# Kernel tuning notes

Measured on AMD Instinct MI355X. Metric: run time of the kernel, lower is better.

Reference implementation:

```python
import jax, jax.numpy as jnp
import numpy as np

N_ITER = 100
EPS = 1e-12


def _corr(x, k):
    # x: [C,H,W], k: [kh,kw]; per-channel 'same' cross-correlation, zero padding
    C = x.shape[0]
    kern = jnp.broadcast_to(k, (C, 1) + k.shape)
    return jax.lax.conv_general_dilated(
        x[None], kern, window_strides=(1, 1), padding='SAME',
        feature_group_count=C,
        dimension_numbers=('NCHW', 'OIHW', 'NCHW'))[0]


def _corr_t(x, k):
    # adjoint of zero-padded 'same' correlation = correlation with flipped kernel
    return _corr(x, k[::-1, ::-1])


def _A(x, kernel, reg_kernels, w2):
    # A x = K^T K x + sum_i w_i^2 R_i^T R_i x
    out = _corr_t(_corr(x, kernel), kernel)
    for i in range(reg_kernels.shape[0]):  # small fixed number of reg kernels
        rk = reg_kernels[i]
        out = out + w2[i] * _corr_t(_corr(x, rk), rk)
    return out


def setup_inputs() -> dict:
    key = jax.random.key(0)
    k1, k2, k3, k4 = jax.random.split(key, 4)
    image = jax.random.uniform(k1, (3, 768, 768), dtype=jnp.float32)
    kernel = jax.random.uniform(k2, (15, 15), dtype=jnp.float32)
    kernel = kernel / jnp.sum(kernel)  # normalized blur PSF
    reg_kernels = jax.random.normal(k3, (2, 5, 5), dtype=jnp.float32)
    reg_kernel_weights = jax.random.uniform(
        k4, (2,), dtype=jnp.float32, minval=1e-6, maxval=1.0)
    return {'image': image, 'kernel': kernel, 'reg_kernels': reg_kernels,
            'reg_kernel_weights': reg_kernel_weights}


def reference(image, kernel, reg_kernels, reg_kernel_weights):
    w2 = reg_kernel_weights ** 2
    # CG init: x0 = image, b = image, solve A x = K^T b
    KTb = _corr_t(image, kernel)
    r0 = KTb - _A(image, kernel, reg_kernels, w2)
    xrp0 = jnp.stack([image, r0, r0])  # [3, C, H, W]: x, r, p

    def body(xrp, _):
        x, r, p = xrp[0], xrp[1], xrp[2]
        Ap = _A(p, kernel, reg_kernels, w2)
        rtr = jnp.sum(r * r, axis=(1, 2), keepdims=True)      # per-channel [C,1,1]
        ptAp = jnp.sum(p * Ap, axis=(1, 2), keepdims=True)
        alpha = rtr / (ptAp + EPS)
        x_new = x + alpha * p
        r_new = r - alpha * Ap
        beta = jnp.sum(r_new * r_new, axis=(1, 2), keepdims=True) / (rtr + EPS)
        p_new = r_new + beta * p
        return jnp.stack([x_new, r_new, p_new]), None

    xrp, _ = jax.lax.scan(jax.checkpoint(body), xrp0, None, length=N_ITER)
    return xrp
```

## Files before the change

kernel.cpp:

```cpp
#include <hip/hip_runtime.h>

#define EPS 1e-12f

constexpr int H = 768, W = 768, C = 3;
constexpr int HW = H * W;
constexpr int CHW = C * HW;

constexpr int NSLOT = 16;
constexpr int SSTR = 16;
constexpr int SCALSZ = NSLOT * SSTR;

constexpr int SPW = 100, SPH = 60;
constexpr int S0W = 84;
constexpr int S1W = 76, S1H = 36;
constexpr int UBUF = SPH * SPW;

constexpr int ESPH = 44;
constexpr int ET0H = 30;
constexpr int ES1H = 20;
constexpr int ELDS = ESPH * SPW + 2 * ES1H * S1W;
constexpr int IPW = 92, IPH = 60;
constexpr int NEDGE = 136;

__device__ __forceinline__ float block_reduce_256(float v, float* redbuf) {
    #pragma unroll
    for (int off = 32; off > 0; off >>= 1) v += __shfl_down(v, off, 64);
    const int tid = threadIdx.x;
    if ((tid & 63) == 0) redbuf[tid >> 6] = v;
    __syncthreads();
    return redbuf[0] + redbuf[1] + redbuf[2] + redbuf[3];
}

__device__ __forceinline__ float sum_slots(const float* base, int c) {
    float s = 0.f;
    #pragma unroll
    for (int k = 0; k < NSLOT; ++k) s += base[k * SSTR + c];
    return s;
}

__global__ void tap_prep_k(const float* __restrict__ k15, const float* __restrict__ rks,
                           const float* __restrict__ rw, float* __restrict__ taps) {
    const int tid = threadIdx.x;
    if (tid < 240) {
        const int i = tid >> 4, j = tid & 15;
        taps[tid]       = (j < 15) ? k15[i * 15 + j] : 0.f;
        taps[240 + tid] = (j < 15) ? k15[(14 - i) * 15 + (14 - j)] : 0.f;
    }
    if (tid < 80) {
        const int kk = tid / 40, rem = tid % 40, i = rem >> 3, j = rem & 7;
        taps[480 + tid] = (j < 5) ? rks[kk * 25 + i * 5 + j] : 0.f;
        taps[560 + tid] = (j < 5) ? rks[kk * 25 + (4 - i) * 5 + (4 - j)] : 0.f;
    }
    const float w20 = rw[0] * rw[0], w21 = rw[1] * rw[1];
    if (tid == 0) { taps[1684] = w20; taps[1685] = w21; }
    for (int t = tid; t < 29 * 36; t += 256) {
        const int uy = t / 36, ux = t - uy * 36;
        float s = 0.f;
        if (ux < 29) {
            const int dy = uy - 14, dx = ux - 14;
            for (int sy = 0; sy < 15; ++sy) {
                const int ty = sy + dy;
                if ((unsigned)ty >= 15u) continue;
                for (int sx = 0; sx < 15; ++sx) {
                    const int tx = sx + dx;
                    if ((unsigned)tx < 15u) s += k15[sy * 15 + sx] * k15[ty * 15 + tx];
                }
            }
            if (dy >= -4 && dy <= 4 && dx >= -4 && dx <= 4) {
                float q0 = 0.f, q1 = 0.f;
                for (int sy = 0; sy < 5; ++sy) {
                    const int ty = sy + dy;
                    if ((unsigned)ty >= 5u) continue;
                    for (int sx = 0; sx < 5; ++sx) {
                        const int tx = sx + dx;
                        if ((unsigned)tx >= 5u) continue;
                        q0 += rks[sy * 5 + sx] * rks[ty * 5 + tx];
                        q1 += rks[25 + sy * 5 + sx] * rks[25 + ty * 5 + tx];
                    }
                }
                s += w20 * q0 + w21 * q1;
            }
        }
        taps[640 + t] = s;
    }
}

__global__ __launch_bounds__(256) void prologue_k(
    const float* __restrict__ img, const float* __restrict__ taps,
    float* __restrict__ outR, float* __restrict__ outP, float* __restrict__ outX,
    float* __restrict__ red)
{
    __shared__ __align__(16) float ub[UBUF];
    __shared__ __align__(16) float st1[S1H * S1W];
    __shared__ __align__(16) float st2[S1H * S1W];
    __shared__ float redbuf[4];

    const float* kt   = taps;
    const float* ktf  = taps + 240;
    const float* rkt  = taps + 480;
    const float* rktf = taps + 560;
    const float w02 = taps[1684], w12 = taps[1685];

    const int c = blockIdx.z;
    const int bx = blockIdx.x * 64, by = blockIdx.y * 32;
    const int tid = threadIdx.x;
    const float* inC = img + c * HW;

    for (int t = tid; t < SPH * 96; t += 256) {
        const int ly = t / 96, lx = t - ly * 96;
        const int gy = by - 14 + ly, gx = bx - 14 + lx;
        float v = 0.f;
        if ((unsigned)gy < (unsigned)H && (unsigned)gx < (unsigned)W) v = inC[gy * W + gx];
        ub[ly * SPW + lx] = v;
    }
    __syncthreads();

    const int oy = tid >> 3;
    const int ox = (tid & 7) << 3;

    {
        const int s0 = tid, s1i = tid + 256;
        const int row0 = s0 / 9, c0 = (s0 - row0 * 9) << 3;
        const int row1 = s1i / 9, c1 = (s1i - row1 * 9) << 3;
        const bool v1 = (s1i < 324);
        float b0[8], c0a[8], b1[8], c1a[8];
        #pragma unroll
        for (int k = 0; k < 8; ++k) { b0[k] = 0.f; c0a[k] = 0.f; b1[k] = 0.f; c1a[k] = 0.f; }
        #pragma unroll 1
        for (int i = 0; i < 5; ++i) {
            float kb[8], kc[8];
            #pragma unroll
            for (int q = 0; q < 2; ++q) {
                *(float4*)(kb + 4 * q) = *(const float4*)(rkt + i * 8 + 4 * q);
                *(float4*)(kc + 4 * q) = *(const float4*)(rkt + 40 + i * 8 + 4 * q);
            }
            {
                const float* rp = ub + (row0 + 10 + i) * SPW + c0 + 8;
                float seg[16];
                #pragma unroll
                for (int q = 0; q < 4; ++q) *(float4*)(seg + 4 * q) = *(const float4*)(rp + 4 * q);
                #pragma unroll
                for (int j = 0; j < 5; ++j)
                    #pragma unroll
                    for (int k = 0; k < 8; ++k) {
                        b0[k]  = fmaf(seg[j + k + 2], kb[j], b0[k]);
                        c0a[k] = fmaf(seg[j + k + 2], kc[j], c0a[k]);
                    }
            }
            if (v1) {
                const float* rp = ub + (row1 + 10 + i) * SPW + c1 + 8;
                float seg[16];
                #pragma unroll
                for (int q = 0; q < 4; ++q) *(float4*)(seg + 4 * q) = *(const float4*)(rp + 4 * q);
                #pragma unroll
                for (int j = 0; j < 5; ++j)
                    #pragma unroll
                    for (int k = 0; k < 8; ++k) {
                        b1[k]  = fmaf(seg[j + k + 2], kb[j], b1[k]);
                        c1a[k] = fmaf(seg[j + k + 2], kc[j], c1a[k]);
                    }
            }
        }
        {
            const int gy = by - 2 + row0, gxb = bx - 2 + c0;
            #pragma unroll
            for (int k = 0; k < 8; ++k)
                if (((unsigned)gy >= (unsigned)H) || ((unsigned)(gxb + k) >= (unsigned)W)) { b0[k] = 0.f; c0a[k] = 0.f; }
            float* o1 = st1 + row0 * S1W + c0;
            float* o2 = st2 + row0 * S1W + c0;
            *(float4*)(o1) = make_float4(b0[0], b0[1], b0[2], b0[3]);
            *(float4*)(o1 + 4) = make_float4(b0[4], b0[5], b0[6], b0[7]);
            *(float4*)(o2) = make_float4(c0a[0], c0a[1], c0a[2], c0a[3]);
            *(float4*)(o2 + 4) = make_float4(c0a[4], c0a[5], c0a[6], c0a[7]);
        }
        if (v1) {
            const int gy = by - 2 + row1, gxb = bx - 2 + c1;
            #pragma unroll
            for (int k = 0; k < 8; ++k)
                if (((unsigned)gy >= (unsigned)H) || ((unsigned)(gxb + k) >= (unsigned)W)) { b1[k] = 0.f; c1a[k] = 0.f; }
            float* o1 = st1 + row1 * S1W + c1;
            float* o2 = st2 + row1 * S1W + c1;
            *(float4*)(o1) = make_float4(b1[0], b1[1], b1[2], b1[3]);
            *(float4*)(o1 + 4) = make_float4(b1[4], b1[5], b1[6], b1[7]);
            *(float4*)(o2) = make_float4(c1a[0], c1a[1], c1a[2], c1a[3]);
            *(float4*)(o2 + 4) = make_float4(c1a[4], c1a[5], c1a[6], c1a[7]);
        }
    }

    float pctr[8];
    {
        const float* ctr = ub + (oy + 14) * SPW + ox + 14;
        #pragma unroll
        for (int k = 0; k < 8; ++k) pctr[k] = ctr[k];
    }

    float vimg[8];
    #pragma unroll
    for (int k = 0; k < 8; ++k) vimg[k] = 0.f;
    #pragma unroll 1
    for (int i = 0; i < 15; ++i) {
        const float* rowp = ub + (oy + 7 + i) * SPW + ox + 4;
        float seg[28];
        #pragma unroll
        for (int q = 0; q < 7; ++q) *(float4*)(seg + 4 * q) = *(const float4*)(rowp + 4 * q);
        float kv[16];
        #pragma unroll
        for (int q = 0; q < 4; ++q) *(float4*)(kv + 4 * q) = *(const float4*)(ktf + i * 16 + 4 * q);
        #pragma unroll
        for (int j = 0; j < 15; ++j)
            #pragma unroll
            for (int k = 0; k < 8; ++k) vimg[k] = fmaf(seg[j + k + 3], kv[j], vimg[k]);
    }

    const int s0 = tid, s1i = tid + 256;
    const int row0 = s0 / 10, ca0 = (s0 - row0 * 10) << 3;
    const int row1 = s1i / 10, ca1 = (s1i - row1 * 10) << 3;
    const bool av1 = (s1i < 460);
    float a0[8], a1[8];
    #pragma unroll
    for (int k = 0; k < 8; ++k) { a0[k] = 0.f; a1[k] = 0.f; }
    #pragma unroll 1
    for (int i = 0; i < 15; ++i) {
        float kv[16];
        #pragma unroll
        for (int q = 0; q < 4; ++q) *(float4*)(kv + 4 * q) = *(const float4*)(kt + i * 16 + 4 * q);
        {
            const float* rp = ub + (row0 + i) * SPW + ca0;
            float seg[24];
            #pragma unroll
            for (int q = 0; q < 6; ++q) *(float4*)(seg + 4 * q) = *(const float4*)(rp + 4 * q);
            #pragma unroll
            for (int j = 0; j < 15; ++j)
                #pragma unroll
                for (int k = 0; k < 8; ++k) a0[k] = fmaf(seg[j + k], kv[j], a0[k]);
        }
        if (av1) {
            const float* rp = ub + (row1 + i) * SPW + ca1;
            float seg[24];
            #pragma unroll
            for (int q = 0; q < 6; ++q) *(float4*)(seg + 4 * q) = *(const float4*)(rp + 4 * q);
            #pragma unroll
            for (int j = 0; j < 15; ++j)
                #pragma unroll
                for (int k = 0; k < 8; ++k) a1[k] = fmaf(seg[j + k], kv[j], a1[k]);
        }
    }
    {
        const int gy = by - 7 + row0, gxb = bx - 7 + ca0;
        #pragma unroll
        for (int k = 0; k < 8; ++k)
            if (((unsigned)gy >= (unsigned)H) || ((unsigned)(gxb + k) >= (unsigned)W)) a0[k] = 0.f;
    }
    if (av1) {
        const int gy = by - 7 + row1, gxb = bx - 7 + ca1;
        #pragma unroll
        for (int k = 0; k < 8; ++k)
            if (((unsigned)gy >= (unsigned)H) || ((unsigned)(gxb + k) >= (unsigned)W)) a1[k] = 0.f;
    }
    __syncthreads();
    {
        float* o = ub + row0 * S0W + ca0;
        *(float4*)(o) = make_float4(a0[0], a0[1], a0[2], a0[3]);
        *(float4*)(o + 4) = make_float4(a0[4], a0[5], a0[6], a0[7]);
    }
    if (av1) {
        float* o = ub + row1 * S0W + ca1;
        *(float4*)(o) = make_float4(a1[0], a1[1], a1[2], a1[3]);
        *(float4*)(o + 4) = make_float4(a1[4], a1[5], a1[6], a1[7]);
    }
    __syncthreads();

    float acc[8];
    #pragma unroll
    for (int k = 0; k < 8; ++k) acc[k] = 0.f;
    #pragma unroll 1
    for (int i = 0; i < 15; ++i) {
        float kv[16];
        #pragma unroll
        for (int q = 0; q < 4; ++q) *(float4*)(kv + 4 * q) = *(const float4*)(ktf + i * 16 + 4 * q);
        const float* rp = ub + (oy + i) * S0W + ox;
        float seg[24];
        #pragma unroll
        for (int q = 0; q < 6; ++q) *(float4*)(seg + 4 * q) = *(const float4*)(rp + 4 * q);
        #pragma unroll
        for (int j = 0; j < 15; ++j)
            #pragma unroll
            for (int k = 0; k < 8; ++k) acc[k] = fmaf(seg[j + k], kv[j], acc[k]);
    }
    float accB[8], accC[8];
    #pragma unroll
    for (int k = 0; k < 8; ++k) { accB[k] = 0.f; accC[k] = 0.f; }
    #pragma unroll 1
    for (int i = 0; i < 5; ++i) {
        float kb[8], kc[8];
        #pragma unroll
        for (int q = 0; q < 2; ++q) {
            *(float4*)(kb + 4 * q) = *(const float4*)(rktf + i * 8 + 4 * q);
            *(float4*)(kc + 4 * q) = *(const float4*)(rktf + 40 + i * 8 + 4 * q);
        }
        const float* r1p = st1 + (oy + i) * S1W + ox;
        const float* r2p = st2 + (oy + i) * S1W + ox;
        float sA[12], sB[12];
        #pragma unroll
        for (int q = 0; q < 3; ++q) *(float4*)(sA + 4 * q) = *(const float4*)(r1p + 4 * q);
        #pragma unroll
        for (int q = 0; q < 3; ++q) *(float4*)(sB + 4 * q) = *(const float4*)(r2p + 4 * q);
        #pragma unroll
        for (int j = 0; j < 5; ++j)
            #pragma unroll
            for (int k = 0; k < 8; ++k) {
                accB[k] = fmaf(sA[j + k], kb[j], accB[k]);
                accC[k] = fmaf(sB[j + k], kc[j], accC[k]);
            }
    }

    float v[8];
    #pragma unroll
    for (int k = 0; k < 8; ++k) v[k] = vimg[k] - (acc[k] + w02 * accB[k] + w12 * accC[k]);

    const int g = c * HW + (by + oy) * W + bx + ox;
    *(float4*)(outR + g)     = make_float4(v[0], v[1], v[2], v[3]);
    *(float4*)(outR + g + 4) = make_float4(v[4], v[5], v[6], v[7]);
    *(float4*)(outP + g)     = make_float4(v[0], v[1], v[2], v[3]);
    *(float4*)(outP + g + 4) = make_float4(v[4], v[5], v[6], v[7]);
    *(float4*)(outX + g)     = make_float4(pctr[0], pctr[1], pctr[2], pctr[3]);
    *(float4*)(outX + g + 4) = make_float4(pctr[4], pctr[5], pctr[6], pctr[7]);
    float local = 0.f;
    #pragma unroll
    for (int k = 0; k < 8; ++k) local += v[k] * v[k];
    const float tot = block_reduce_256(local, redbuf);
    if (tid == 0) {
        const int bid = blockIdx.y * gridDim.x + blockIdx.x;
        atomicAdd(red + (bid & (NSLOT - 1)) * SSTR + c, tot);
    }
}

template <bool FIRST>
__global__ __launch_bounds__(256) void stepA_k(
    const float* __restrict__ pold, const float* __restrict__ rvec,
    const float* __restrict__ taps,
    float* __restrict__ Apnew, float* __restrict__ pnew,
    const float* __restrict__ rtrI, const float* __restrict__ rtrIm1,
    float* __restrict__ ptapI)
{
    __shared__ __align__(16) float lds[ELDS];
    __shared__ float redbuf[4];
    const int c = blockIdx.z;
    const int tid = threadIdx.x;
    const int bid = blockIdx.x;

    float beta = 0.f;
    if (!FIRST) beta = sum_slots(rtrI, c) / (sum_slots(rtrIm1, c) + EPS);

    float S1 = 0.f;

    if (bid < NEDGE) {
        float* ub  = lds;
        float* st1 = lds + ESPH * SPW;
        float* st2 = st1 + ES1H * S1W;
        const float* kt   = taps;
        const float* ktf  = taps + 240;
        const float* rkt  = taps + 480;
        const float* rktf = taps + 560;
        const float w02 = taps[1684], w12 = taps[1685];

        const int e = bid >> 1, half = bid & 1;
        int tbx, tby;
        { if (e < 12)      { tbx = e;      tby = 0; }
          else if (e < 24) { tbx = e - 12; tby = 23; }
          else if (e < 46) { tbx = 0;      tby = 1 + (e - 24); }
          else             { tbx = 11;     tby = 1 + (e - 46); } }
        const int bx = tbx * 64, by = tby * 32 + half * 16;

        for (int s = tid; s < ESPH * 96; s += 256) {
            const int ly = s / 96, lx = s - ly * 96;
            const int gy = by - 14 + ly, gx = bx - 14 + lx;
            float pe = 0.f;
            if ((unsigned)gy < (unsigned)H && (unsigned)gx < (unsigned)W) {
                const int g = c * HW + gy * W + gx;
                const float pv = pold[g];
                if (FIRST) pe = pv;
                else {
                    pe = fmaf(beta, pv, rvec[g]);
                    if (ly >= 14 && ly < 30 && lx >= 14 && lx < 78) pnew[g] = pe;
                }
            }
            ub[ly * SPW + lx] = pe;
        }
        __syncthreads();

        const int oy2 = tid >> 4;
        const int ox2 = (tid & 15) << 2;

        {
            const int row0 = tid / 9, c0 = (tid - (tid / 9) * 9) << 3;
            const bool act = (tid < 180);
            float b0[8], c0a[8];
            #pragma unroll
            for (int k = 0; k < 8; ++k) { b0[k] = 0.f; c0a[k] = 0.f; }
            if (act) {
                #pragma unroll 1
                for (int i = 0; i < 5; ++i) {
                    float kb[8], kc[8];
                    #pragma unroll
                    for (int q = 0; q < 2; ++q) {
                        *(float4*)(kb + 4 * q) = *(const float4*)(rkt + i * 8 + 4 * q);
                        *(float4*)(kc + 4 * q) = *(const float4*)(rkt + 40 + i * 8 + 4 * q);
                    }
                    const float* rp = ub + (row0 + 10 + i) * SPW + c0 + 8;
                    float seg[16];
                    #pragma unroll
                    for (int q = 0; q < 4; ++q) *(float4*)(seg + 4 * q) = *(const float4*)(rp + 4 * q);
                    #pragma unroll
                    for (int j = 0; j < 5; ++j)
                        #pragma unroll
                        for (int k = 0; k < 8; ++k) {
                            b0[k]  = fmaf(seg[j + k + 2], kb[j], b0[k]);
                            c0a[k] = fmaf(seg[j + k + 2], kc[j], c0a[k]);
                        }
                }
                const int gy = by - 2 + row0, gxb = bx - 2 + c0;
                #pragma unroll
                for (int k = 0; k < 8; ++k)
                    if (((unsigned)gy >= (unsigned)H) || ((unsigned)(gxb + k) >= (unsigned)W)) { b0[k] = 0.f; c0a[k] = 0.f; }
                float* o1 = st1 + row0 * S1W + c0;
                float* o2 = st2 + row0 * S1W + c0;
                *(float4*)(o1) = make_float4(b0[0], b0[1], b0[2], b0[3]);
                *(float4*)(o1 + 4) = make_float4(b0[4], b0[5], b0[6], b0[7]);
                *(float4*)(o2) = make_float4(c0a[0], c0a[1], c0a[2], c0a[3]);
                *(float4*)(o2 + 4) = make_float4(c0a[4], c0a[5], c0a[6], c0a[7]);
            }
        }

        float pctr[4];
        {
            const float* ctr = ub + (oy2 + 14) * SPW + ox2 + 14;
            #pragma unroll
            for (int k = 0; k < 4; ++k) pctr[k] = ctr[k];
        }

        const int s0 = tid, s1i = tid + 256;
        const int row0 = s0 / 10, ca0 = (s0 - row0 * 10) << 3;
        const int row1 = s1i / 10, ca1 = (s1i - row1 * 10) << 3;
        const bool av1 = (s1i < 300);
        float a0[8], a1[8];
        #pragma unroll
        for (int k = 0; k < 8; ++k) { a0[k] = 0.f; a1[k] = 0.f; }
        #pragma unroll 1
        for (int i = 0; i < 15; ++i) {
            float kv[16];
            #pragma unroll
            for (int q = 0; q < 4; ++q) *(float4*)(kv + 4 * q) = *(const float4*)(kt + i * 16 + 4 * q);
            {
                const float* rp = ub + (row0 + i) * SPW + ca0;
                float seg[24];
                #pragma unroll
                for (int q = 0; q < 6; ++q) *(float4*)(seg + 4 * q) = *(const float4*)(rp + 4 * q);
                #pragma unroll
                for (int j = 0; j < 15; ++j)
                    #pragma unroll
                    for (int k = 0; k < 8; ++k) a0[k] = fmaf(seg[j + k], kv[j], a0[k]);
            }
            if (av1) {
                const float* rp = ub + (row1 + i) * SPW + ca1;
                float seg[24];
                #pragma unroll
                for (int q = 0; q < 6; ++q) *(float4*)(seg + 4 * q) = *(const float4*)(rp + 4 * q);
                #pragma unroll
                for (int j = 0; j < 15; ++j)
                    #pragma unroll
                    for (int k = 0; k < 8; ++k) a1[k] = fmaf(seg[j + k], kv[j], a1[k]);
            }
        }
        {
            const int gy = by - 7 + row0, gxb = bx - 7 + ca0;
            #pragma unroll
            for (int k = 0; k < 8; ++k)
                if (((unsigned)gy >= (unsigned)H) || ((unsigned)(gxb + k) >= (unsigned)W)) a0[k] = 0.f;
        }
        if (av1) {
            const int gy = by - 7 + row1, gxb = bx - 7 + ca1;
            #pragma unroll
            for (int k = 0; k < 8; ++k)
                if (((unsigned)gy >= (unsigned)H) || ((unsigned)(gxb + k) >= (unsigned)W)) a1[k] = 0.f;
        }
        __syncthreads();
        {
            float* o = ub + row0 * S0W + ca0;
            *(float4*)(o) = make_float4(a0[0], a0[1], a0[2], a0[3]);
            *(float4*)(o + 4) = make_float4(a0[4], a0[5], a0[6], a0[7]);
        }
        if (av1) {
            float* o = ub + row1 * S0W + ca1;
            *(float4*)(o) = make_float4(a1[0], a1[1], a1[2], a1[3]);
            *(float4*)(o + 4) = make_float4(a1[4], a1[5], a1[6], a1[7]);
        }
        __syncthreads();

        float acc[4];
        #pragma unroll
        for (int k = 0; k < 4; ++k) acc[k] = 0.f;
        #pragma unroll 1
        for (int i = 0; i < 15; ++i) {
            float kv[16];
            #pragma unroll
            for (int q = 0; q < 4; ++q) *(float4*)(kv + 4 * q) = *(const float4*)(ktf + i * 16 + 4 * q);
            const float* rp = ub + (oy2 + i) * S0W + ox2;
            float seg[20];
            #pragma unroll
            for (int q = 0; q < 5; ++q) *(float4*)(seg + 4 * q) = *(const float4*)(rp + 4 * q);
            #pragma unroll
            for (int j = 0; j < 15; ++j)
                #pragma unroll
                for (int k = 0; k < 4; ++k) acc[k] = fmaf(seg[j + k], kv[j], acc[k]);
        }
        float accB[4], accC[4];
        #pragma unroll
        for (int k = 0; k < 4; ++k) { accB[k] = 0.f; accC[k] = 0.f; }
        #pragma unroll 1
        for (int i = 0; i < 5; ++i) {
            float kb[8], kc[8];
            #pragma unroll
            for (int q = 0; q < 2; ++q) {
                *(float4*)(kb + 4 * q) = *(const float4*)(rktf + i * 8 + 4 * q);
                *(float4*)(kc + 4 * q) = *(const float4*)(rktf + 40 + i * 8 + 4 * q);
            }
            const float* r1p = st1 + (oy2 + i) * S1W + ox2;
            const float* r2p = st2 + (oy2 + i) * S1W + ox2;
            float sA[8], sB[8];
            #pragma unroll
            for (int q = 0; q < 2; ++q) *(float4*)(sA + 4 * q) = *(const float4*)(r1p + 4 * q);
            #pragma unroll
            for (int q = 0; q < 2; ++q) *(float4*)(sB + 4 * q) = *(const float4*)(r2p + 4 * q);
            #pragma unroll
            for (int j = 0; j < 5; ++j)
                #pragma unroll
                for (int k = 0; k < 4; ++k) {
                    accB[k] = fmaf(sA[j + k], kb[j], accB[k]);
                    accC[k] = fmaf(sB[j + k], kc[j], accC[k]);
                }
        }

        float v[4];
        #pragma unroll
        for (int k = 0; k < 4; ++k) v[k] = acc[k] + w02 * accB[k] + w12 * accC[k];

        const int g = c * HW + (by + oy2) * W + bx + ox2;
        *(float4*)(Apnew + g) = make_float4(v[0], v[1], v[2], v[3]);
        #pragma unroll
        for (int k = 0; k < 4; ++k) S1 += pctr[k] * v[k];
    } else {
        const float* tk = taps + 640;
        const int b = bid - NEDGE;
        const int bx = 64 + (b % 10) * 64, by = 32 + (b / 10) * 32;
        const int gy0 = by - 14, gx0 = bx - 14;

        for (int s = tid; s < IPH * IPW; s += 256) {
            const int ly = s / IPW, lx = s - ly * IPW;
            const int g = c * HW + (gy0 + ly) * W + (gx0 + lx);
            const float pv = pold[g];
            float pe;
            if (FIRST) pe = pv;
            else {
                pe = fmaf(beta, pv, rvec[g]);
                if (ly >= 14 && ly < 46 && lx >= 14 && lx < 78) pnew[g] = pe;
            }
            lds[s] = pe;
        }
        __syncthreads();

        const int ox = (tid & 15) << 2;
        const int o0 = (tid >> 4) << 1;

        float a0[4], a1[4];
        #pragma unroll
        for (int k = 0; k < 4; ++k) { a0[k] = 0.f; a1[k] = 0.f; }
        {
            const float* rp = lds + o0 * IPW + ox;
            float seg[32];
            #pragma unroll
            for (int q = 0; q < 8; ++q) *(float4*)(seg + 4 * q) = *(const float4*)(rp + 4 * q);
            #pragma unroll
            for (int j = 0; j < 29; ++j) {
                const float kv = tk[j];
                #pragma unroll
                for (int k = 0; k < 4; ++k) a0[k] = fmaf(seg[j + k], kv, a0[k]);
            }
        }
        #pragma unroll 1
        for (int d = 1; d <= 28; ++d) {
            const float* rp = lds + (o0 + d) * IPW + ox;
            float seg[32];
            #pragma unroll
            for (int q = 0; q < 8; ++q) *(float4*)(seg + 4 * q) = *(const float4*)(rp + 4 * q);
            const float* kr0 = tk + d * 36;
            const float* kr1 = kr0 - 36;
            #pragma unroll
            for (int j = 0; j < 29; ++j) {
                const float kv0 = kr0[j], kv1 = kr1[j];
                #pragma unroll
                for (int k = 0; k < 4; ++k) {
                    a0[k] = fmaf(seg[j + k], kv0, a0[k]);
                    a1[k] = fmaf(seg[j + k], kv1, a1[k]);
                }
            }
        }
        {
            const float* rp = lds + (o0 + 29) * IPW + ox;
            float seg[32];
            #pragma unroll
            for (int q = 0; q < 8; ++q) *(float4*)(seg + 4 * q) = *(const float4*)(rp + 4 * q);
            const float* kr1 = tk + 28 * 36;
            #pragma unroll
            for (int j = 0; j < 29; ++j) {
                const float kv = kr1[j];
                #pragma unroll
                for (int k = 0; k < 4; ++k) a1[k] = fmaf(seg[j + k], kv, a1[k]);
            }
        }

        const int gbase = c * HW + (by + o0) * W + bx + ox;
        const float* c0p = lds + (o0 + 14) * IPW + ox + 14;
        const float* c1p = c0p + IPW;
        *(float4*)(Apnew + gbase)     = make_float4(a0[0], a0[1], a0[2], a0[3]);
        *(float4*)(Apnew + gbase + W) = make_float4(a1[0], a1[1], a1[2], a1[3]);
        #pragma unroll
        for (int k = 0; k < 4; ++k) S1 += c0p[k] * a0[k] + c1p[k] * a1[k];
    }

    const float tot = block_reduce_256(S1, redbuf);
    if (tid == 0) atomicAdd(ptapI + (bid & (NSLOT - 1)) * SSTR + c, tot);
}

__global__ __launch_bounds__(256) void cgr_k(
    float* __restrict__ r, const float* __restrict__ Ap,
    float* __restrict__ x, const float* __restrict__ p,
    const float* __restrict__ rtrI, const float* __restrict__ ptapI,
    float* __restrict__ rtrNext)
{
    __shared__ float redbuf[4];
    const int c = blockIdx.z;
    const float alpha = sum_slots(rtrI, c) / (sum_slots(ptapI, c) + EPS);
    const int idx = c * HW + (blockIdx.x * 256 + threadIdx.x) * 8;
    float local = 0.f;
    #pragma unroll
    for (int h = 0; h < 2; ++h) {
        const int o = idx + 4 * h;
        float4 rv = *(float4*)(r + o);
        float4 xv = *(float4*)(x + o);
        const float4 av = *(const float4*)(Ap + o);
        const float4 pv = *(const float4*)(p + o);
        rv.x = fmaf(-alpha, av.x, rv.x); xv.x = fmaf(alpha, pv.x, xv.x);
        rv.y = fmaf(-alpha, av.y, rv.y); xv.y = fmaf(alpha, pv.y, xv.y);
        rv.z = fmaf(-alpha, av.z, rv.z); xv.z = fmaf(alpha, pv.z, xv.z);
        rv.w = fmaf(-alpha, av.w, rv.w); xv.w = fmaf(alpha, pv.w, xv.w);
        *(float4*)(r + o) = rv;
        *(float4*)(x + o) = xv;
        local += rv.x * rv.x + rv.y * rv.y + rv.z * rv.z + rv.w * rv.w;
    }
    const float tot = block_reduce_256(local, redbuf);
    if (threadIdx.x == 0)
        atomicAdd(rtrNext + ((int)blockIdx.x & (NSLOT - 1)) * SSTR + c, tot);
}

__global__ __launch_bounds__(256) void ep_k(
    const float* __restrict__ r100, const float* __restrict__ p99, float* __restrict__ pout,
    const float* __restrict__ rtr99s, const float* __restrict__ rtr100s)
{
    const int c = blockIdx.z;
    const float beta = sum_slots(rtr100s, c) / (sum_slots(rtr99s, c) + EPS);
    const int idx = c * HW + (blockIdx.x * 256 + threadIdx.x) * 8;
    #pragma unroll
    for (int h = 0; h < 2; ++h) {
        const int o = idx + 4 * h;
        const float4 pv = *(const float4*)(p99 + o);
        const float4 rv = *(const float4*)(r100 + o);
        *(float4*)(pout + o) = make_float4(
            fmaf(beta, pv.x, rv.x), fmaf(beta, pv.y, rv.y),
            fmaf(beta, pv.z, rv.z), fmaf(beta, pv.w, rv.w));
    }
}

extern "C" void kernel_launch(void* const* d_in, const int* in_sizes, int n_in,
                              void* d_out, int out_size, void* d_ws, size_t ws_size,
                              hipStream_t stream)
{
    const float* img = (const float*)d_in[0];
    const float* k15 = (const float*)d_in[1];
    const float* rks = (const float*)d_in[2];
    const float* rw  = (const float*)d_in[3];

    float* out = (float*)d_out;
    float* xs = out;
    float* rs = out + CHW;
    float* ps = out + 2 * CHW;

    float* ws = (float*)d_ws;
    float* pA   = ws;
    float* pB   = ws + CHW;
    float* Ap   = ws + 2 * CHW;
    float* scal = ws + 3 * CHW;
    float* rtrS  = scal;
    float* ptapS = scal + 101 * SCALSZ;
    float* taps  = scal + 201 * SCALSZ;

    float* pbuf[2] = { pA, pB };

    hipMemsetAsync(scal, 0, (size_t)201 * SCALSZ * sizeof(float), stream);
    tap_prep_k<<<1, 256, 0, stream>>>(k15, rks, rw, taps);

    const dim3 bc(256);
    prologue_k<<<dim3(12, 24, 3), bc, 0, stream>>>(img, taps, rs, pA, xs, rtrS);

    for (int i = 0; i < 100; ++i) {
        float* pcur;
        if (i == 0) {
            pcur = pA;
            stepA_k<true><<<dim3(NEDGE + 220, 1, 3), bc, 0, stream>>>(
                pA, rs, taps, Ap, nullptr, rtrS, rtrS, ptapS);
        } else {
            pcur = pbuf[i & 1];
            stepA_k<false><<<dim3(NEDGE + 220, 1, 3), bc, 0, stream>>>(
                pbuf[(i - 1) & 1], rs, taps, Ap, pcur,
                rtrS + (size_t)i * SCALSZ, rtrS + (size_t)(i - 1) * SCALSZ,
                ptapS + (size_t)i * SCALSZ);
        }
        cgr_k<<<dim3(288, 1, 3), bc, 0, stream>>>(
            rs, Ap, xs, pcur,
            rtrS + (size_t)i * SCALSZ, ptapS + (size_t)i * SCALSZ,
            rtrS + (size_t)(i + 1) * SCALSZ);
    }
    ep_k<<<dim3(288, 1, 3), bc, 0, stream>>>(
        rs, pB, ps, rtrS + (size_t)99 * SCALSZ, rtrS + (size_t)100 * SCALSZ);
}
```

Measured before the change: 8.736 ms.

## Fuse CG iterations into a persistent cooperative kernel with grid syncs

The 200 per-iteration launches (convolution step plus CG update) are replaced by a single cooperative kernel that loops over all 100 iterations, with grid-wide barriers between the phases. Block-to-work mapping is flattened into a 1D grid that covers edge tiles, interior tiles and channels. The aim is to remove kernel-launch and drain gaps between the many short dependent kernels. In exchange it adds grid-sync cost, and `__launch_bounds__(256,5)` caps register use, which risks spills in the heavy convolution code. A non-cooperative fallback path is kept.

```diff
diff --git a/kernel.cpp b/kernel.cpp
--- a/kernel.cpp
+++ b/kernel.cpp
@@ -1,4 +1,7 @@
 #include <hip/hip_runtime.h>
+#include <hip/hip_cooperative_groups.h>
+
+namespace cg = cooperative_groups;
 
 #define EPS 1e-12f
 
@@ -16,11 +19,12 @@
 constexpr int UBUF = SPH * SPW;
 
 constexpr int ESPH = 44;
-constexpr int ET0H = 30;
 constexpr int ES1H = 20;
 constexpr int ELDS = ESPH * SPW + 2 * ES1H * S1W;
 constexpr int IPW = 92, IPH = 60;
-constexpr int NEDGE = 136;
+constexpr int NEDGE3 = 408;
+constexpr int NGRID = 1068;
+constexpr int NB_B = 864;
 
 __device__ __forceinline__ float block_reduce_256(float v, float* redbuf) {
     #pragma unroll
@@ -335,26 +339,24 @@
     }
 }
 
-template <bool FIRST>
-__global__ __launch_bounds__(256) void stepA_k(
-    const float* __restrict__ pold, const float* __restrict__ rvec,
-    const float* __restrict__ taps,
-    float* __restrict__ Apnew, float* __restrict__ pnew,
-    const float* __restrict__ rtrI, const float* __restrict__ rtrIm1,
-    float* __restrict__ ptapI)
+
+__device__ __forceinline__ void phaseA_body(
+    int bid, int tid, float* lds, float* redbuf, bool first,
+    const float* __restrict__ pold, const float* __restrict__ rvec, float* __restrict__ pnew,
+    const float* __restrict__ taps, float* __restrict__ Ap,
+    const float* __restrict__ rtrI, const float* __restrict__ rtrIm1, float* __restrict__ ptapI)
 {
-    __shared__ __align__(16) float lds[ELDS];
-    __shared__ float redbuf[4];
-    const int c = blockIdx.z;
-    const int tid = threadIdx.x;
-    const int bid = blockIdx.x;
+    const bool is_edge = (bid < NEDGE3);
+    int c, rb;
+    if (is_edge) { c = bid % 3; rb = bid / 3; }
+    else { const int v = bid - NEDGE3; c = v % 3; rb = v / 3; }
 
     float beta = 0.f;
-    if (!FIRST) beta = sum_slots(rtrI, c) / (sum_slots(rtrIm1, c) + EPS);
+    if (!first) beta = sum_slots(rtrI, c) / (sum_slots(rtrIm1, c) + EPS);
 
     float S1 = 0.f;
 
-    if (bid < NEDGE) {
+    if (is_edge) {
         float* ub  = lds;
         float* st1 = lds + ESPH * SPW;
         float* st2 = st1 + ES1H * S1W;
@@ -364,7 +366,7 @@
         const float* rktf = taps + 560;
         const float w02 = taps[1684], w12 = taps[1685];
 
-        const int e = bid >> 1, half = bid & 1;
+        const int e = rb >> 1, half = rb & 1;
         int tbx, tby;
         { if (e < 12)      { tbx = e;      tby = 0; }
           else if (e < 24) { tbx = e - 12; tby = 23; }
@@ -379,7 +381,7 @@
             if ((unsigned)gy < (unsigned)H && (unsigned)gx < (unsigned)W) {
                 const int g = c * HW + gy * W + gx;
                 const float pv = pold[g];
-                if (FIRST) pe = pv;
+                if (first) pe = pv;
                 else {
                     pe = fmaf(beta, pv, rvec[g]);
                     if (ly >= 14 && ly < 30 && lx >= 14 && lx < 78) pnew[g] = pe;
@@ -394,20 +396,19 @@
 
         {
             const int row0 = tid / 9, c0 = (tid - (tid / 9) * 9) << 3;
-            const bool act = (tid < 180);
-            float b0[8], c0a[8];
-            #pragma unroll
-            for (int k = 0; k < 8; ++k) { b0[k] = 0.f; c0a[k] = 0.f; }
-            if (act) {
+            if (tid < 180) {
+                float b0[8], c0a[8];
+                #pragma unroll
+                for (int k = 0; k < 8; ++k) { b0[k] = 0.f; c0a[k] = 0.f; }
                 #pragma unroll 1
-                for (int i = 0; i < 5; ++i) {
+                for (int ii = 0; ii < 5; ++ii) {
                     float kb[8], kc[8];
                     #pragma unroll
                     for (int q = 0; q < 2; ++q) {
-                        *(float4*)(kb + 4 * q) = *(const float4*)(rkt + i * 8 + 4 * q);
-                        *(float4*)(kc + 4 * q) = *(const float4*)(rkt + 40 + i * 8 + 4 * q);
+                        *(float4*)(kb + 4 * q) = *(const float4*)(rkt + ii * 8 + 4 * q);
+                        *(float4*)(kc + 4 * q) = *(const float4*)(rkt + 40 + ii * 8 + 4 * q);
                     }
-                    const float* rp = ub + (row0 + 10 + i) * SPW + c0 + 8;
+                    const float* rp = ub + (row0 + 10 + ii) * SPW + c0 + 8;
                     float seg[16];
                     #pragma unroll
                     for (int q = 0; q < 4; ++q) *(float4*)(seg + 4 * q) = *(const float4*)(rp + 4 * q);
@@ -447,12 +448,12 @@
         #pragma unroll
         for (int k = 0; k < 8; ++k) { a0[k] = 0.f; a1[k] = 0.f; }
         #pragma unroll 1
-        for (int i = 0; i < 15; ++i) {
+        for (int ii = 0; ii < 15; ++ii) {
             float kv[16];
             #pragma unroll
-            for (int q = 0; q < 4; ++q) *(float4*)(kv + 4 * q) = *(const float4*)(kt + i * 16 + 4 * q);
+            for (int q = 0; q < 4; ++q) *(float4*)(kv + 4 * q) = *(const float4*)(kt + ii * 16 + 4 * q);
             {
-                const float* rp = ub + (row0 + i) * SPW + ca0;
+                const float* rp = ub + (row0 + ii) * SPW + ca0;
                 float seg[24];
                 #pragma unroll
                 for (int q = 0; q < 6; ++q) *(float4*)(seg + 4 * q) = *(const float4*)(rp + 4 * q);
@@ -462,7 +463,7 @@
                     for (int k = 0; k < 8; ++k) a0[k] = fmaf(seg[j + k], kv[j], a0[k]);
             }
             if (av1) {
-                const float* rp = ub + (row1 + i) * SPW + ca1;
+                const float* rp = ub + (row1 + ii) * SPW + ca1;
                 float seg[24];
                 #pragma unroll
                 for (int q = 0; q < 6; ++q) *(float4*)(seg + 4 * q) = *(const float4*)(rp + 4 * q);
@@ -501,11 +502,11 @@
         #pragma unroll
         for (int k = 0; k < 4; ++k) acc[k] = 0.f;
         #pragma unroll 1
-        for (int i = 0; i < 15; ++i) {
+        for (int ii = 0; ii < 15; ++ii) {
             float kv[16];
             #pragma unroll
-            for (int q = 0; q < 4; ++q) *(float4*)(kv + 4 * q) = *(const float4*)(ktf + i * 16 + 4 * q);
-            const float* rp = ub + (oy2 + i) * S0W + ox2;
+            for (int q = 0; q < 4; ++q) *(float4*)(kv + 4 * q) = *(const float4*)(ktf + ii * 16 + 4 * q);
+            const float* rp = ub + (oy2 + ii) * S0W + ox2;
             float seg[20];
             #pragma unroll
             for (int q = 0; q < 5; ++q) *(float4*)(seg + 4 * q) = *(const float4*)(rp + 4 * q);
@@ -518,15 +519,15 @@
         #pragma unroll
         for (int k = 0; k < 4; ++k) { accB[k] = 0.f; accC[k] = 0.f; }
         #pragma unroll 1
-        for (int i = 0; i < 5; ++i) {
+        for (int ii = 0; ii < 5; ++ii) {
             float kb[8], kc[8];
             #pragma unroll
             for (int q = 0; q < 2; ++q) {
-                *(float4*)(kb + 4 * q) = *(const float4*)(rktf + i * 8 + 4 * q);
-                *(float4*)(kc + 4 * q) = *(const float4*)(rktf + 40 + i * 8 + 4 * q);
-            }
-            const float* r1p = st1 + (oy2 + i) * S1W + ox2;
-            const float* r2p = st2 + (oy2 + i) * S1W + ox2;
+                *(float4*)(kb + 4 * q) = *(const float4*)(rktf + ii * 8 + 4 * q);
+                *(float4*)(kc + 4 * q) = *(const float4*)(rktf + 40 + ii * 8 + 4 * q);
+            }
+            const float* r1p = st1 + (oy2 + ii) * S1W + ox2;
+            const float* r2p = st2 + (oy2 + ii) * S1W + ox2;
             float sA[8], sB[8];
             #pragma unroll
             for (int q = 0; q < 2; ++q) *(float4*)(sA + 4 * q) = *(const float4*)(r1p + 4 * q);
@@ -546,13 +547,12 @@
         for (int k = 0; k < 4; ++k) v[k] = acc[k] + w02 * accB[k] + w12 * accC[k];
 
         const int g = c * HW + (by + oy2) * W + bx + ox2;
-        *(float4*)(Apnew + g) = make_float4(v[0], v[1], v[2], v[3]);
+        *(float4*)(Ap + g) = make_float4(v[0], v[1], v[2], v[3]);
         #pragma unroll
         for (int k = 0; k < 4; ++k) S1 += pctr[k] * v[k];
     } else {
         const float* tk = taps + 640;
-        const int b = bid - NEDGE;
-        const int bx = 64 + (b % 10) * 64, by = 32 + (b / 10) * 32;
+        const int bx = 64 + (rb % 10) * 64, by = 32 + (rb / 10) * 32;
         const int gy0 = by - 14, gx0 = bx - 14;
 
         for (int s = tid; s < IPH * IPW; s += 256) {
@@ -560,7 +560,7 @@
             const int g = c * HW + (gy0 + ly) * W + (gx0 + lx);
             const float pv = pold[g];
             float pe;
-            if (FIRST) pe = pv;
+            if (first) pe = pv;
             else {
                 pe = fmaf(beta, pv, rvec[g]);
                 if (ly >= 14 && ly < 46 && lx >= 14 && lx < 78) pnew[g] = pe;
@@ -622,8 +622,8 @@
         const int gbase = c * HW + (by + o0) * W + bx + ox;
         const float* c0p = lds + (o0 + 14) * IPW + ox + 14;
         const float* c1p = c0p + IPW;
-        *(float4*)(Apnew + gbase)     = make_float4(a0[0], a0[1], a0[2], a0[3]);
-        *(float4*)(Apnew + gbase + W) = make_float4(a1[0], a1[1], a1[2], a1[3]);
+        *(float4*)(Ap + gbase)     = make_float4(a0[0], a0[1], a0[2], a0[3]);
+        *(float4*)(Ap + gbase + W) = make_float4(a1[0], a1[1], a1[2], a1[3]);
         #pragma unroll
         for (int k = 0; k < 4; ++k) S1 += c0p[k] * a0[k] + c1p[k] * a1[k];
     }
@@ -632,53 +632,110 @@
     if (tid == 0) atomicAdd(ptapI + (bid & (NSLOT - 1)) * SSTR + c, tot);
 }
 
-__global__ __launch_bounds__(256) void cgr_k(
-    float* __restrict__ r, const float* __restrict__ Ap,
-    float* __restrict__ x, const float* __restrict__ p,
+__device__ __forceinline__ void phaseB_body(
+    int bid, int tid, float* redbuf,
+    float* __restrict__ r, float* __restrict__ x,
+    const float* __restrict__ Ap, const float* __restrict__ pc,
     const float* __restrict__ rtrI, const float* __restrict__ ptapI,
     float* __restrict__ rtrNext)
 {
-    __shared__ float redbuf[4];
-    const int c = blockIdx.z;
-    const float alpha = sum_slots(rtrI, c) / (sum_slots(ptapI, c) + EPS);
-    const int idx = c * HW + (blockIdx.x * 256 + threadIdx.x) * 8;
+    const int c3 = bid / 288;
+    const float alpha = sum_slots(rtrI, c3) / (sum_slots(ptapI, c3) + EPS);
+    const int o = (bid * 256 + tid) * 8;
     float local = 0.f;
     #pragma unroll
     for (int h = 0; h < 2; ++h) {
-        const int o = idx + 4 * h;
-        float4 rv = *(float4*)(r + o);
-        float4 xv = *(float4*)(x + o);
-        const float4 av = *(const float4*)(Ap + o);
-        const float4 pv = *(const float4*)(p + o);
+        const int oo = o + 4 * h;
+        float4 rv = *(float4*)(r + oo);
+        float4 xv = *(float4*)(x + oo);
+        const float4 av = *(const float4*)(Ap + oo);
+        const float4 pv = *(const float4*)(pc + oo);
         rv.x = fmaf(-alpha, av.x, rv.x); xv.x = fmaf(alpha, pv.x, xv.x);
         rv.y = fmaf(-alpha, av.y, rv.y); xv.y = fmaf(alpha, pv.y, xv.y);
         rv.z = fmaf(-alpha, av.z, rv.z); xv.z = fmaf(alpha, pv.z, xv.z);
         rv.w = fmaf(-alpha, av.w, rv.w); xv.w = fmaf(alpha, pv.w, xv.w);
-        *(float4*)(r + o) = rv;
-        *(float4*)(x + o) = xv;
+        *(float4*)(r + oo) = rv;
+        *(float4*)(x + oo) = xv;
         local += rv.x * rv.x + rv.y * rv.y + rv.z * rv.z + rv.w * rv.w;
     }
     const float tot = block_reduce_256(local, redbuf);
-    if (threadIdx.x == 0)
-        atomicAdd(rtrNext + ((int)blockIdx.x & (NSLOT - 1)) * SSTR + c, tot);
-}
-
-__global__ __launch_bounds__(256) void ep_k(
+    if (tid == 0)
+        atomicAdd(rtrNext + (bid & (NSLOT - 1)) * SSTR + c3, tot);
+}
+
+__device__ __forceinline__ void epilogue_body(
+    int bid, int tid,
     const float* __restrict__ r100, const float* __restrict__ p99, float* __restrict__ pout,
     const float* __restrict__ rtr99s, const float* __restrict__ rtr100s)
 {
-    const int c = blockIdx.z;
-    const float beta = sum_slots(rtr100s, c) / (sum_slots(rtr99s, c) + EPS);
-    const int idx = c * HW + (blockIdx.x * 256 + threadIdx.x) * 8;
+    const int c3 = bid / 288;
+    const float beta = sum_slots(rtr100s, c3) / (sum_slots(rtr99s, c3) + EPS);
+    const int o = (bid * 256 + tid) * 8;
     #pragma unroll
     for (int h = 0; h < 2; ++h) {
-        const int o = idx + 4 * h;
-        const float4 pv = *(const float4*)(p99 + o);
-        const float4 rv = *(const float4*)(r100 + o);
-        *(float4*)(pout + o) = make_float4(
+        const int oo = o + 4 * h;
+        const float4 pv = *(const float4*)(p99 + oo);
+        const float4 rv = *(const float4*)(r100 + oo);
+        *(float4*)(pout + oo) = make_float4(
             fmaf(beta, pv.x, rv.x), fmaf(beta, pv.y, rv.y),
             fmaf(beta, pv.z, rv.z), fmaf(beta, pv.w, rv.w));
     }
+}
+
+__global__ __launch_bounds__(256, 5) void cg_coop_k(
+    float* r, float* x, float* pA, float* pB, float* Ap,
+    const float* taps, float* rtrS, float* ptapS, float* pout)
+{
+    cg::grid_group grid = cg::this_grid();
+    __shared__ __align__(16) float lds[ELDS];
+    __shared__ float redbuf[4];
+    const int bid = blockIdx.x;
+    const int tid = threadIdx.x;
+
+    for (int i = 0; i < 100; ++i) {
+        const bool first = (i == 0);
+        const float* rtrI = rtrS + (size_t)i * SCALSZ;
+        float* ptapI = ptapS + (size_t)i * SCALSZ;
+        const float* pold = first ? pA : ((i & 1) ? pA : pB);
+        float* pnew = (i & 1) ? pB : pA;
+
+        phaseA_body(bid, tid, lds, redbuf, first, pold, r, pnew, taps, Ap,
+                    rtrI, rtrI - SCALSZ, ptapI);
+        grid.sync();
+        if (bid < NB_B)
+            phaseB_body(bid, tid, redbuf, r, x, Ap, first ? pA : pnew,
+                        rtrI, ptapI, rtrS + (size_t)(i + 1) * SCALSZ);
+        grid.sync();
+    }
+    if (bid < NB_B)
+        epilogue_body(bid, tid, r, pB, pout,
+                      rtrS + (size_t)99 * SCALSZ, rtrS + (size_t)100 * SCALSZ);
+}
+
+__global__ __launch_bounds__(256) void stepA_sk(
+    int first, const float* pold, const float* rvec, float* pnew,
+    const float* taps, float* Ap,
+    const float* rtrI, const float* rtrIm1, float* ptapI)
+{
+    __shared__ __align__(16) float lds[ELDS];
+    __shared__ float redbuf[4];
+    phaseA_body(blockIdx.x, threadIdx.x, lds, redbuf, first != 0,
+                pold, rvec, pnew, taps, Ap, rtrI, rtrIm1, ptapI);
+}
+
+__global__ __launch_bounds__(256) void cgr_sk(
+    float* r, float* x, const float* Ap, const float* pc,
+    const float* rtrI, const float* ptapI, float* rtrNext)
+{
+    __shared__ float redbuf[4];
+    phaseB_body(blockIdx.x, threadIdx.x, redbuf, r, x, Ap, pc, rtrI, ptapI, rtrNext);
+}
+
+__global__ __launch_bounds__(256) void ep_sk(
+    const float* r100, const float* p99, float* pout,
+    const float* rtr99s, const float* rtr100s)
+{
+    epilogue_body(blockIdx.x, threadIdx.x, r100, p99, pout, rtr99s, rtr100s);
 }
 
 extern "C" void kernel_launch(void* const* d_in, const int* in_sizes, int n_in,
@@ -704,32 +761,40 @@
     float* ptapS = scal + 101 * SCALSZ;
     float* taps  = scal + 201 * SCALSZ;
 
-    float* pbuf[2] = { pA, pB };
-
     hipMemsetAsync(scal, 0, (size_t)201 * SCALSZ * sizeof(float), stream);
     tap_prep_k<<<1, 256, 0, stream>>>(k15, rks, rw, taps);
 
     const dim3 bc(256);
     prologue_k<<<dim3(12, 24, 3), bc, 0, stream>>>(img, taps, rs, pA, xs, rtrS);
 
-    for (int i = 0; i < 100; ++i) {
-        float* pcur;
-        if (i == 0) {
-            pcur = pA;
-            stepA_k<true><<<dim3(NEDGE + 220, 1, 3), bc, 0, stream>>>(
-                pA, rs, taps, Ap, nullptr, rtrS, rtrS, ptapS);
-        } else {
-            pcur = pbuf[i & 1];
-            stepA_k<false><<<dim3(NEDGE + 220, 1, 3), bc, 0, stream>>>(
-                pbuf[(i - 1) & 1], rs, taps, Ap, pcur,
-                rtrS + (size_t)i * SCALSZ, rtrS + (size_t)(i - 1) * SCALSZ,
-                ptapS + (size_t)i * SCALSZ);
-        }
-        cgr_k<<<dim3(288, 1, 3), bc, 0, stream>>>(
-            rs, Ap, xs, pcur,
-            rtrS + (size_t)i * SCALSZ, ptapS + (size_t)i * SCALSZ,
-            rtrS + (size_t)(i + 1) * SCALSZ);
-    }
-    ep_k<<<dim3(288, 1, 3), bc, 0, stream>>>(
-        rs, pB, ps, rtrS + (size_t)99 * SCALSZ, rtrS + (size_t)100 * SCALSZ);
-}
+    int maxb = 0;
+    (void)hipOccupancyMaxActiveBlocksPerMultiprocessor(&maxb, cg_coop_k, 256, 0);
+    const bool coop_ok = (maxb * 256 >= NGRID);
+
+    if (coop_ok) {
+        void* kargs[] = { (void*)&rs, (void*)&xs, (void*)&pA, (void*)&pB, (void*)&Ap,
+                          (void*)&taps, (void*)&rtrS, (void*)&ptapS, (void*)&ps };
+        hipLaunchCooperativeKernel((const void*)cg_coop_k, dim3(NGRID), bc, kargs, 0, stream);
+    } else {
+        float* pbuf[2] = { pA, pB };
+        for (int i = 0; i < 100; ++i) {
+            const float* rtrI = rtrS + (size_t)i * SCALSZ;
+            float* ptapI = ptapS + (size_t)i * SCALSZ;
+            float* pcur;
+            if (i == 0) {
+                pcur = pA;
+                stepA_sk<<<dim3(NGRID), bc, 0, stream>>>(
+                    1, pA, rs, nullptr, taps, Ap, rtrI, rtrI, ptapI);
+            } else {
+                pcur = pbuf[i & 1];
+                stepA_sk<<<dim3(NGRID), bc, 0, stream>>>(
+                    0, pbuf[(i - 1) & 1], rs, pcur, taps, Ap,
+                    rtrI, rtrS + (size_t)(i - 1) * SCALSZ, ptapI);
+            }
+            cgr_sk<<<dim3(NB_B), bc, 0, stream>>>(
+                rs, xs, Ap, pcur, rtrI, ptapI, rtrS + (size_t)(i + 1) * SCALSZ);
+        }
+        ep_sk<<<dim3(NB_B), bc, 0, stream>>>(
+            rs, pB, ps, rtrS + (size_t)99 * SCALSZ, rtrS + (size_t)100 * SCALSZ);
+    }
+}
```

New measurement: 8.724 ms. Within noise of the previous version (-0.1%).
